# Optimization experiments

Measured on AMD Instinct MI355X. Metric: run time of the kernel, lower is better.

## Reference

```python
import jax, jax.numpy as jnp
import numpy as np

N = 8192
QS = 128
KS = 128
F = 256
EPS = 1e-5     # BatchNorm1d default eps
SLOPE = 0.01   # LeakyReLU default negative_slope


def _leaky(x):
    return jnp.where(x >= 0, x, SLOPE * x)


def _mlp_bn(x, w1, b1, w2, b2, gamma, beta):
    # Sequential(Linear, LeakyReLU, Linear, LeakyReLU) then BatchNorm1d (training mode)
    h = _leaky(x @ w1 + b1)
    h = _leaky(h @ w2 + b2)
    mean = h.mean(axis=0)
    var = h.var(axis=0)  # biased variance, as torch BN uses for normalization
    return gamma * (h - mean) * jax.lax.rsqrt(var + EPS) + beta


def setup_inputs() -> dict:
    key = jax.random.key(0)
    ks = jax.random.split(key, 24)

    def lin_w(k_, fi, fo):
        s = 1.0 / np.sqrt(fi)
        return jax.random.uniform(k_, (fi, fo), minval=-s, maxval=s, dtype=jnp.float32)

    def lin_b(k_, fi, fo):
        s = 1.0 / np.sqrt(fi)
        return jax.random.uniform(k_, (fo,), minval=-s, maxval=s, dtype=jnp.float32)

    A = (jax.random.uniform(ks[0], (N, N)) < 0.004).astype(jnp.float32)
    q = jax.random.normal(ks[1], (N, QS), dtype=jnp.float32)
    k = jax.random.normal(ks[2], (N, KS), dtype=jnp.float32)

    inp = {"A": A, "q": q, "k": k}
    i = 3
    for pre, fi in (("q", QS), ("k", KS), ("v", KS)):
        inp[pre + "_w1"] = lin_w(ks[i], fi, F); i += 1
        inp[pre + "_b1"] = lin_b(ks[i], fi, F); i += 1
        inp[pre + "_w2"] = lin_w(ks[i], F, F); i += 1
        inp[pre + "_b2"] = lin_b(ks[i], F, F); i += 1
        inp[pre + "_gamma"] = jnp.ones((F,), jnp.float32)
        inp[pre + "_beta"] = jnp.zeros((F,), jnp.float32)
    return inp


def reference(A, q, k,
              q_w1, q_b1, q_w2, q_b2, q_gamma, q_beta,
              k_w1, k_b1, k_w2, k_b2, k_gamma, k_beta,
              v_w1, v_b1, v_w2, v_b2, v_gamma, v_beta):
    qe1 = _mlp_bn(q, q_w1, q_b1, q_w2, q_b2, q_gamma, q_beta)   # [N, F]
    ke1 = _mlp_bn(k, k_w1, k_b1, k_w2, k_b2, k_gamma, k_beta)   # [N, F]
    prod = (qe1 @ ke1.T) / jnp.sqrt(jnp.float32(F))             # [N, N]
    # NOTE: faithful to source — mask zeroes scores (not -inf) before softmax
    masked = A * prod
    attn = jax.nn.softmax(masked, axis=1)
    ve1 = _mlp_bn(k, v_w1, v_b1, v_w2, v_b2, v_gamma, v_beta)   # [N, F]
    return attn @ ve1                                            # [N, F]
```

## Files before the change

kernel.cpp:

```cpp
#include <hip/hip_runtime.h>

#define NROWS 8192
#define FDIM 256
#define CAP 128

typedef _Float16 half8_t __attribute__((ext_vector_type(8)));
typedef _Float16 half4_t __attribute__((ext_vector_type(4)));
typedef float floatx4 __attribute__((ext_vector_type(4)));

struct MlpPtrs {
  const float* w1[3]; const float* b1[3];
  const float* w2[3]; const float* b2[3];
  const float* gamma[3]; const float* beta[3];
};

__global__ __launch_bounds__(256) void prep_kernel(
    const float* __restrict__ q, const float* __restrict__ k, MlpPtrs p,
    _Float16* __restrict__ qh, _Float16* __restrict__ kh,
    _Float16* __restrict__ w1p, _Float16* __restrict__ w2p) {
  int task = blockIdx.y;
  int tid = blockIdx.x * 256 + threadIdx.x;
  if (task < 2) {
    const float* src = task == 0 ? q : k;
    _Float16* dst = task == 0 ? qh : kh;
    const floatx4* s4 = (const floatx4*)src;
    half4_t* d4 = (half4_t*)dst;
    for (int idx = tid; idx < (NROWS * 128) / 4; idx += 256 * 256) {
      floatx4 v = s4[idx];
      d4[idx] = (half4_t){(_Float16)v[0], (_Float16)v[1], (_Float16)v[2], (_Float16)v[3]};
    }
    return;
  }
  int m = (task - 2) % 3;
  bool isw2 = task >= 5;
  int K = isw2 ? 256 : 128;
  if (tid >= K * 256) return;
  const float* src = isw2 ? p.w2[m] : p.w1[m];
  _Float16* dst = isw2 ? (w2p + m * 65536) : (w1p + m * 32768);
  int j = tid & 7, lane = (tid >> 3) & 63, rest = tid >> 9;
  int ktiles = K >> 5;
  int k_tile = rest % ktiles, n_tile = rest / ktiles;
  int kk = k_tile * 32 + (lane >> 4) * 8 + j;
  int nn = n_tile * 16 + (lane & 15);
  dst[tid] = (_Float16)src[kk * 256 + nn];
}

__global__ __launch_bounds__(256) void gemm1_kernel(
    const _Float16* __restrict__ qh, const _Float16* __restrict__ kh,
    const _Float16* __restrict__ w1p, MlpPtrs p, _Float16* __restrict__ h1) {
  const int mlp = blockIdx.z;
  const _Float16* X = (mlp == 0) ? qh : kh;
  const _Float16* wp = w1p + mlp * 32768;
  _Float16* out = h1 + (size_t)mlp * (NROWS * FDIM);
  const float* bias = p.b1[mlp];
  int lane = threadIdx.x & 63, wave = threadIdx.x >> 6;
  int lm = lane & 15, lq = lane >> 4;
  int m0 = blockIdx.x * 64 + wave * 16;
  int n0 = blockIdx.y * 64;
  floatx4 acc[4];
  #pragma unroll
  for (int t = 0; t < 4; ++t) acc[t] = (floatx4){0.f, 0.f, 0.f, 0.f};
  const half8_t* ap = (const half8_t*)(X + (size_t)(m0 + lm) * 128 + lq * 8);
  const half8_t* wp8 = (const half8_t*)wp;
  #pragma unroll
  for (int kt = 0; kt < 4; ++kt) {
    half8_t a = ap[kt * 4];
    #pragma unroll
    for (int t = 0; t < 4; ++t) {
      half8_t b = wp8[(((n0 >> 4) + t) * 4 + kt) * 64 + lane];
      acc[t] = __builtin_amdgcn_mfma_f32_16x16x32_f16(a, b, acc[t], 0, 0, 0);
    }
  }
  #pragma unroll
  for (int t = 0; t < 4; ++t) {
    int col = n0 + t * 16 + lm;
    float bb = bias[col];
    #pragma unroll
    for (int r = 0; r < 4; ++r) {
      float v = acc[t][r] + bb;
      v = (v >= 0.f) ? v : 0.01f * v;
      out[(size_t)(m0 + lq * 4 + r) * FDIM + col] = (_Float16)v;
    }
  }
}

__global__ __launch_bounds__(256) void gemm2_kernel(
    const _Float16* __restrict__ h1, const _Float16* __restrict__ w2p,
    MlpPtrs p, _Float16* __restrict__ e1,
    float* __restrict__ colsum, float* __restrict__ colsumsq) {
  const int mlp = blockIdx.z;
  const _Float16* X = h1 + (size_t)mlp * (NROWS * FDIM);
  const _Float16* wp = w2p + mlp * 65536;
  _Float16* out = e1 + (size_t)mlp * (NROWS * FDIM);
  const float* bias = p.b2[mlp];
  int lane = threadIdx.x & 63, wave = threadIdx.x >> 6;
  int lm = lane & 15, lq = lane >> 4;
  int m0 = blockIdx.x * 64 + wave * 16;
  int n0 = blockIdx.y * 64;
  floatx4 acc[4];
  #pragma unroll
  for (int t = 0; t < 4; ++t) acc[t] = (floatx4){0.f, 0.f, 0.f, 0.f};
  const half8_t* ap = (const half8_t*)(X + (size_t)(m0 + lm) * 256 + lq * 8);
  const half8_t* wp8 = (const half8_t*)wp;
  #pragma unroll
  for (int kt = 0; kt < 8; ++kt) {
    half8_t a = ap[kt * 4];
    #pragma unroll
    for (int t = 0; t < 4; ++t) {
      half8_t b = wp8[(((n0 >> 4) + t) * 8 + kt) * 64 + lane];
      acc[t] = __builtin_amdgcn_mfma_f32_16x16x32_f16(a, b, acc[t], 0, 0, 0);
    }
  }
  #pragma unroll
  for (int t = 0; t < 4; ++t) {
    int col = n0 + t * 16 + lm;
    float bb = bias[col];
    float s = 0.f, s2 = 0.f;
    #pragma unroll
    for (int r = 0; r < 4; ++r) {
      float v = acc[t][r] + bb;
      v = (v >= 0.f) ? v : 0.01f * v;
      out[(size_t)(m0 + lq * 4 + r) * FDIM + col] = (_Float16)v;
      s += v; s2 += v * v;
    }
    s  += __shfl_xor(s, 16, 64);  s  += __shfl_xor(s, 32, 64);
    s2 += __shfl_xor(s2, 16, 64); s2 += __shfl_xor(s2, 32, 64);
    if (lq == 0) {
      atomicAdd(&colsum[mlp * FDIM + col], s);
      atomicAdd(&colsumsq[mlp * FDIM + col], s2);
    }
  }
}

__global__ __launch_bounds__(256) void norm_kernel(
    _Float16* __restrict__ e1, const float* __restrict__ colsum,
    const float* __restrict__ colsumsq, MlpPtrs p, float* __restrict__ S_all) {
  int mlp = blockIdx.y;
  int c = threadIdx.x;
  _Float16* h = e1 + (size_t)mlp * (NROWS * FDIM);
  float mean = colsum[mlp * FDIM + c] * (1.f / NROWS);
  float var = colsumsq[mlp * FDIM + c] * (1.f / NROWS) - mean * mean;
  float scale = p.gamma[mlp][c] * rsqrtf(var + 1e-5f);
  float shift = p.beta[mlp][c] - mean * scale;
  int r0 = blockIdx.x * 32;
  float sv = 0.f;
  for (int r = 0; r < 32; ++r) {
    size_t idx = (size_t)(r0 + r) * FDIM + c;
    float v = (float)h[idx] * scale + shift;
    _Float16 hv = (_Float16)v;
    h[idx] = hv;
    sv += (float)hv;
  }
  if (mlp == 2) atomicAdd(&S_all[c], sv);
}

__global__ __launch_bounds__(256) void attn_kernel(
    const float* __restrict__ A,
    const _Float16* __restrict__ e1, const float* __restrict__ S_all,
    float* __restrict__ out) {
  const _Float16* qe = e1;
  const _Float16* ke = e1 + (size_t)1 * NROWS * FDIM;
  const _Float16* ve = e1 + (size_t)2 * NROWS * FDIM;
  int i = blockIdx.x;
  int tid = threadIdx.x, lane = tid & 63, wave = tid >> 6;
  __shared__ int sj[CAP];
  __shared__ float sw[CAP];
  __shared__ float pacc[4][FDIM];
  __shared__ int s_cnt;
  if (tid == 0) s_cnt = 0;
  __syncthreads();

  const floatx4* row = (const floatx4*)(A + (size_t)i * NROWS);
  floatx4 av[8];
  #pragma unroll
  for (int it = 0; it < 8; ++it)
    av[it] = __builtin_nontemporal_load(&row[it * 256 + tid]);
  #pragma unroll
  for (int it = 0; it < 8; ++it) {
    int v4 = it * 256 + tid;
    int cols[4]; int c = 0;
    if (av[it][0] != 0.f) cols[c++] = v4 * 4 + 0;
    if (av[it][1] != 0.f) cols[c++] = v4 * 4 + 1;
    if (av[it][2] != 0.f) cols[c++] = v4 * 4 + 2;
    if (av[it][3] != 0.f) cols[c++] = v4 * 4 + 3;
    if (c) {
      int pos = atomicAdd(&s_cnt, c);
      for (int l = 0; l < c; ++l) if (pos + l < CAP) sj[pos + l] = cols[l];
    }
  }
  __syncthreads();
  int nnz = s_cnt < CAP ? s_cnt : CAP;

  int cl = lane & 15, g = lane >> 4;
  const half8_t* qe8 = (const half8_t*)(qe + (size_t)i * FDIM + cl * 16);
  half8_t qa = qe8[0], qb = qe8[1];
  for (int e = wave * 4 + g; e < nnz; e += 16) {
    int j = sj[e];
    const half8_t* ke8 = (const half8_t*)(ke + (size_t)j * FDIM + cl * 16);
    half8_t ka = ke8[0], kb = ke8[1];
    float s = 0.f;
    #pragma unroll
    for (int r = 0; r < 8; ++r)
      s += (float)qa[r] * (float)ka[r] + (float)qb[r] * (float)kb[r];
    #pragma unroll
    for (int off = 8; off >= 1; off >>= 1) s += __shfl_xor(s, off, 64);
    if (cl == 0) sw[e] = s * 0.0625f;
  }
  __syncthreads();

  float v0 = lane < nnz ? sw[lane] : 0.f;
  float v1 = lane + 64 < nnz ? sw[lane + 64] : 0.f;
  float m = fmaxf(fmaxf(v0, v1), 0.f);
  #pragma unroll
  for (int off = 32; off >= 1; off >>= 1) m = fmaxf(m, __shfl_xor(m, off, 64));
  float em = __expf(-m);
  float w0 = lane < nnz ? __expf(v0 - m) : 0.f;
  float w1 = lane + 64 < nnz ? __expf(v1 - m) : 0.f;
  float ls = w0 + w1;
  #pragma unroll
  for (int off = 32; off >= 1; off >>= 1) ls += __shfl_xor(ls, off, 64);
  float inv = 1.f / (ls + (float)(NROWS - nnz) * em);

  int par = lane >> 5, c8 = lane & 31;
  floatx4 accA = (floatx4){0.f, 0.f, 0.f, 0.f};
  floatx4 accB = (floatx4){0.f, 0.f, 0.f, 0.f};
  for (int e = wave * 2 + par; e < nnz; e += 8) {
    int j = sj[e];
    float w = __expf(sw[e] - m) - em;
    half8_t vv = *(const half8_t*)(ve + (size_t)j * FDIM + c8 * 8);
    accA[0] += w * (float)vv[0]; accA[1] += w * (float)vv[1];
    accA[2] += w * (float)vv[2]; accA[3] += w * (float)vv[3];
    accB[0] += w * (float)vv[4]; accB[1] += w * (float)vv[5];
    accB[2] += w * (float)vv[6]; accB[3] += w * (float)vv[7];
  }
  #pragma unroll
  for (int r = 0; r < 4; ++r) {
    accA[r] += __shfl_xor(accA[r], 32, 64);
    accB[r] += __shfl_xor(accB[r], 32, 64);
  }
  if (par == 0) {
    ((floatx4*)&pacc[wave][c8 * 8])[0] = accA;
    ((floatx4*)&pacc[wave][c8 * 8])[1] = accB;
  }
  __syncthreads();

  int c = tid;
  float s = pacc[0][c] + pacc[1][c] + pacc[2][c] + pacc[3][c] + em * S_all[c];
  __builtin_nontemporal_store(s * inv, &out[(size_t)i * FDIM + c]);
}

extern "C" void kernel_launch(void* const* d_in, const int* in_sizes, int n_in,
                              void* d_out, int out_size, void* d_ws, size_t ws_size,
                              hipStream_t stream) {
  const float* A = (const float*)d_in[0];
  const float* q = (const float*)d_in[1];
  const float* k = (const float*)d_in[2];
  MlpPtrs p;
  for (int m = 0; m < 3; ++m) {
    const int b = 3 + m * 6;
    p.w1[m]    = (const float*)d_in[b + 0];
    p.b1[m]    = (const float*)d_in[b + 1];
    p.w2[m]    = (const float*)d_in[b + 2];
    p.b2[m]    = (const float*)d_in[b + 3];
    p.gamma[m] = (const float*)d_in[b + 4];
    p.beta[m]  = (const float*)d_in[b + 5];
  }
  char* ws = (char*)d_ws;
  const size_t MB = 1024 * 1024;
  _Float16* qh  = (_Float16*)(ws + 0);
  _Float16* kh  = (_Float16*)(ws + 2 * MB);
  _Float16* h1  = (_Float16*)(ws + 4 * MB);
  _Float16* e1  = (_Float16*)(ws + 16 * MB);
  _Float16* w1p = (_Float16*)(ws + 28 * MB);
  _Float16* w2p = (_Float16*)(ws + 28 * MB + 192 * 1024);
  float* colsum   = (float*)(ws + 28 * MB + 640 * 1024);
  float* colsumsq = colsum + 3 * FDIM;
  float* S_all    = colsumsq + 3 * FDIM;

  (void)hipMemsetAsync(colsum, 0, 7 * 1024, stream);
  prep_kernel<<<dim3(256, 8, 1), 256, 0, stream>>>(q, k, p, qh, kh, w1p, w2p);
  gemm1_kernel<<<dim3(128, 4, 3), 256, 0, stream>>>(qh, kh, w1p, p, h1);
  gemm2_kernel<<<dim3(128, 4, 3), 256, 0, stream>>>(h1, w2p, p, e1, colsum, colsumsq);
  norm_kernel<<<dim3(256, 3, 1), 256, 0, stream>>>(e1, colsum, colsumsq, p, S_all);
  attn_kernel<<<NROWS, 256, 0, stream>>>(A, e1, S_all, (float*)d_out);
}
```

Baseline: 458.0 us.

## Fold BatchNorm affine into attention and assign one row per wave

Drops the separate norm pass that rewrote all three embeddings. Instead a tiny stats kernel computes per-column scale and shift, which the attention kernel applies algebraically: scaled q times k-scale in the score, and v's affine applied after aggregation using colsum. The fp32-to-fp16 conversion of q and k moves into gemm1's loads, removing the staging copy. Attention now processes one row per wave with no block-level syncs. This trades extra per-row arithmetic and fp16-rounding differences from unnormalized values for less memory traffic and fewer launches.

After: 456.0 us (median of 2 runs). No clear change (-0.4%).

```diff
diff --git a/kernel.cpp b/kernel.cpp
--- a/kernel.cpp
+++ b/kernel.cpp
@@ -15,24 +15,11 @@
 };
 
 __global__ __launch_bounds__(256) void prep_kernel(
-    const float* __restrict__ q, const float* __restrict__ k, MlpPtrs p,
-    _Float16* __restrict__ qh, _Float16* __restrict__ kh,
-    _Float16* __restrict__ w1p, _Float16* __restrict__ w2p) {
+    MlpPtrs p, _Float16* __restrict__ w1p, _Float16* __restrict__ w2p) {
   int task = blockIdx.y;
   int tid = blockIdx.x * 256 + threadIdx.x;
-  if (task < 2) {
-    const float* src = task == 0 ? q : k;
-    _Float16* dst = task == 0 ? qh : kh;
-    const floatx4* s4 = (const floatx4*)src;
-    half4_t* d4 = (half4_t*)dst;
-    for (int idx = tid; idx < (NROWS * 128) / 4; idx += 256 * 256) {
-      floatx4 v = s4[idx];
-      d4[idx] = (half4_t){(_Float16)v[0], (_Float16)v[1], (_Float16)v[2], (_Float16)v[3]};
-    }
-    return;
-  }
-  int m = (task - 2) % 3;
-  bool isw2 = task >= 5;
+  int m = task % 3;
+  bool isw2 = task >= 3;
   int K = isw2 ? 256 : 128;
   if (tid >= K * 256) return;
   const float* src = isw2 ? p.w2[m] : p.w1[m];
@@ -46,10 +33,10 @@
 }
 
 __global__ __launch_bounds__(256) void gemm1_kernel(
-    const _Float16* __restrict__ qh, const _Float16* __restrict__ kh,
+    const float* __restrict__ q, const float* __restrict__ k,
     const _Float16* __restrict__ w1p, MlpPtrs p, _Float16* __restrict__ h1) {
   const int mlp = blockIdx.z;
-  const _Float16* X = (mlp == 0) ? qh : kh;
+  const float* X = (mlp == 0) ? q : k;
   const _Float16* wp = w1p + mlp * 32768;
   _Float16* out = h1 + (size_t)mlp * (NROWS * FDIM);
   const float* bias = p.b1[mlp];
@@ -60,11 +47,14 @@
   floatx4 acc[4];
   #pragma unroll
   for (int t = 0; t < 4; ++t) acc[t] = (floatx4){0.f, 0.f, 0.f, 0.f};
-  const half8_t* ap = (const half8_t*)(X + (size_t)(m0 + lm) * 128 + lq * 8);
+  const float* ap = X + (size_t)(m0 + lm) * 128 + lq * 8;
   const half8_t* wp8 = (const half8_t*)wp;
   #pragma unroll
   for (int kt = 0; kt < 4; ++kt) {
-    half8_t a = ap[kt * 4];
+    floatx4 a0 = *(const floatx4*)(ap + kt * 32);
+    floatx4 a1 = *(const floatx4*)(ap + kt * 32 + 4);
+    half8_t a = (half8_t){(_Float16)a0[0], (_Float16)a0[1], (_Float16)a0[2], (_Float16)a0[3],
+                          (_Float16)a1[0], (_Float16)a1[1], (_Float16)a1[2], (_Float16)a1[3]};
     #pragma unroll
     for (int t = 0; t < 4; ++t) {
       half8_t b = wp8[(((n0 >> 4) + t) * 4 + kt) * 64 + lane];
@@ -132,84 +122,92 @@
   }
 }
 
-__global__ __launch_bounds__(256) void norm_kernel(
-    _Float16* __restrict__ e1, const float* __restrict__ colsum,
-    const float* __restrict__ colsumsq, MlpPtrs p, float* __restrict__ S_all) {
-  int mlp = blockIdx.y;
+__global__ __launch_bounds__(256) void stats_kernel(
+    const float* __restrict__ colsum, const float* __restrict__ colsumsq,
+    MlpPtrs p, float* __restrict__ scaleA, float* __restrict__ shiftA) {
   int c = threadIdx.x;
-  _Float16* h = e1 + (size_t)mlp * (NROWS * FDIM);
-  float mean = colsum[mlp * FDIM + c] * (1.f / NROWS);
-  float var = colsumsq[mlp * FDIM + c] * (1.f / NROWS) - mean * mean;
-  float scale = p.gamma[mlp][c] * rsqrtf(var + 1e-5f);
-  float shift = p.beta[mlp][c] - mean * scale;
-  int r0 = blockIdx.x * 32;
-  float sv = 0.f;
-  for (int r = 0; r < 32; ++r) {
-    size_t idx = (size_t)(r0 + r) * FDIM + c;
-    float v = (float)h[idx] * scale + shift;
-    _Float16 hv = (_Float16)v;
-    h[idx] = hv;
-    sv += (float)hv;
-  }
-  if (mlp == 2) atomicAdd(&S_all[c], sv);
+  #pragma unroll
+  for (int m = 0; m < 3; ++m) {
+    float mean = colsum[m * FDIM + c] * (1.f / NROWS);
+    float var = colsumsq[m * FDIM + c] * (1.f / NROWS) - mean * mean;
+    float sc = p.gamma[m][c] * rsqrtf(var + 1e-5f);
+    scaleA[m * FDIM + c] = sc;
+    shiftA[m * FDIM + c] = p.beta[m][c] - mean * sc;
+  }
 }
 
 __global__ __launch_bounds__(256) void attn_kernel(
-    const float* __restrict__ A,
-    const _Float16* __restrict__ e1, const float* __restrict__ S_all,
-    float* __restrict__ out) {
+    const float* __restrict__ A, const _Float16* __restrict__ e1,
+    const float* __restrict__ scaleA, const float* __restrict__ shiftA,
+    const float* __restrict__ colsum, float* __restrict__ out) {
   const _Float16* qe = e1;
   const _Float16* ke = e1 + (size_t)1 * NROWS * FDIM;
   const _Float16* ve = e1 + (size_t)2 * NROWS * FDIM;
-  int i = blockIdx.x;
-  int tid = threadIdx.x, lane = tid & 63, wave = tid >> 6;
-  __shared__ int sj[CAP];
-  __shared__ float sw[CAP];
-  __shared__ float pacc[4][FDIM];
-  __shared__ int s_cnt;
-  if (tid == 0) s_cnt = 0;
-  __syncthreads();
+  int lane = threadIdx.x & 63, wave = threadIdx.x >> 6;
+  int i = blockIdx.x * 4 + wave;
+  __shared__ int sj[4][CAP];
+  __shared__ float sw[4][CAP];
+  __shared__ int cnt[4];
+  if (lane == 0) cnt[wave] = 0;
 
   const floatx4* row = (const floatx4*)(A + (size_t)i * NROWS);
-  floatx4 av[8];
-  #pragma unroll
-  for (int it = 0; it < 8; ++it)
-    av[it] = __builtin_nontemporal_load(&row[it * 256 + tid]);
-  #pragma unroll
-  for (int it = 0; it < 8; ++it) {
-    int v4 = it * 256 + tid;
-    int cols[4]; int c = 0;
-    if (av[it][0] != 0.f) cols[c++] = v4 * 4 + 0;
-    if (av[it][1] != 0.f) cols[c++] = v4 * 4 + 1;
-    if (av[it][2] != 0.f) cols[c++] = v4 * 4 + 2;
-    if (av[it][3] != 0.f) cols[c++] = v4 * 4 + 3;
-    if (c) {
-      int pos = atomicAdd(&s_cnt, c);
-      for (int l = 0; l < c; ++l) if (pos + l < CAP) sj[pos + l] = cols[l];
-    }
-  }
-  __syncthreads();
-  int nnz = s_cnt < CAP ? s_cnt : CAP;
+  for (int b = 0; b < 4; ++b) {
+    floatx4 av[8];
+    #pragma unroll
+    for (int it = 0; it < 8; ++it)
+      av[it] = __builtin_nontemporal_load(&row[(b * 8 + it) * 64 + lane]);
+    #pragma unroll
+    for (int it = 0; it < 8; ++it) {
+      int base = ((b * 8 + it) * 64 + lane) * 4;
+      int cols[4]; int c = 0;
+      if (av[it][0] != 0.f) cols[c++] = base + 0;
+      if (av[it][1] != 0.f) cols[c++] = base + 1;
+      if (av[it][2] != 0.f) cols[c++] = base + 2;
+      if (av[it][3] != 0.f) cols[c++] = base + 3;
+      if (c) {
+        int pos = atomicAdd(&cnt[wave], c);
+        for (int l = 0; l < c; ++l) if (pos + l < CAP) sj[wave][pos + l] = cols[l];
+      }
+    }
+  }
+  int nnz = cnt[wave] < CAP ? cnt[wave] : CAP;
 
   int cl = lane & 15, g = lane >> 4;
-  const half8_t* qe8 = (const half8_t*)(qe + (size_t)i * FDIM + cl * 16);
-  half8_t qa = qe8[0], qb = qe8[1];
-  for (int e = wave * 4 + g; e < nnz; e += 16) {
-    int j = sj[e];
-    const half8_t* ke8 = (const half8_t*)(ke + (size_t)j * FDIM + cl * 16);
-    half8_t ka = ke8[0], kb = ke8[1];
-    float s = 0.f;
+  const half8_t* qp = (const half8_t*)(qe + (size_t)i * FDIM + cl * 16);
+  half8_t qa = qp[0], qb8 = qp[1];
+  const floatx4* sq4 = (const floatx4*)(scaleA + cl * 16);
+  const floatx4* hq4 = (const floatx4*)(shiftA + cl * 16);
+  const floatx4* sk4 = (const floatx4*)(scaleA + FDIM + cl * 16);
+  const floatx4* hk4 = (const floatx4*)(shiftA + FDIM + cl * 16);
+  float qk[16]; float qb = 0.f;
+  #pragma unroll
+  for (int v4 = 0; v4 < 4; ++v4) {
+    floatx4 sq = sq4[v4], hq = hq4[v4], sk = sk4[v4], hk = hk4[v4];
+    #pragma unroll
+    for (int r = 0; r < 4; ++r) {
+      int c = v4 * 4 + r;
+      float qr = (c < 8) ? (float)qa[c] : (float)qb8[c - 8];
+      float qn = qr * sq[r] + hq[r];
+      qk[c] = qn * sk[r] * 0.0625f;
+      qb += qn * hk[r] * 0.0625f;
+    }
+  }
+
+  for (int e = g; e < nnz; e += 4) {
+    int j = sj[wave][e];
+    const half8_t* kp = (const half8_t*)(ke + (size_t)j * FDIM + cl * 16);
+    half8_t ka = kp[0], kb = kp[1];
+    float s = qb;
     #pragma unroll
     for (int r = 0; r < 8; ++r)
-      s += (float)qa[r] * (float)ka[r] + (float)qb[r] * (float)kb[r];
+      s += qk[r] * (float)ka[r] + qk[r + 8] * (float)kb[r];
     #pragma unroll
     for (int off = 8; off >= 1; off >>= 1) s += __shfl_xor(s, off, 64);
-    if (cl == 0) sw[e] = s * 0.0625f;
-  }
-  __syncthreads();
-
-  float v0 = lane < nnz ? sw[lane] : 0.f;
-  float v1 = lane + 64 < nnz ? sw[lane + 64] : 0.f;
+    if (cl == 0) sw[wave][e] = s;
+  }
+
+  float v0 = lane < nnz ? sw[wave][lane] : 0.f;
+  float v1 = lane + 64 < nnz ? sw[wave][lane + 64] : 0.f;
   float m = fmaxf(fmaxf(v0, v1), 0.f);
   #pragma unroll
   for (int off = 32; off >= 1; off >>= 1) m = fmaxf(m, __shfl_xor(m, off, 64));
@@ -219,34 +217,29 @@
   float ls = w0 + w1;
   #pragma unroll
   for (int off = 32; off >= 1; off >>= 1) ls += __shfl_xor(ls, off, 64);
+  if (lane < nnz) sw[wave][lane] = w0 - em;
+  if (lane + 64 < nnz) sw[wave][lane + 64] = w1 - em;
+  float wsum = ls - (float)nnz * em;
   float inv = 1.f / (ls + (float)(NROWS - nnz) * em);
 
-  int par = lane >> 5, c8 = lane & 31;
-  floatx4 accA = (floatx4){0.f, 0.f, 0.f, 0.f};
-  floatx4 accB = (floatx4){0.f, 0.f, 0.f, 0.f};
-  for (int e = wave * 2 + par; e < nnz; e += 8) {
-    int j = sj[e];
-    float w = __expf(sw[e] - m) - em;
-    half8_t vv = *(const half8_t*)(ve + (size_t)j * FDIM + c8 * 8);
-    accA[0] += w * (float)vv[0]; accA[1] += w * (float)vv[1];
-    accA[2] += w * (float)vv[2]; accA[3] += w * (float)vv[3];
-    accB[0] += w * (float)vv[4]; accB[1] += w * (float)vv[5];
-    accB[2] += w * (float)vv[6]; accB[3] += w * (float)vv[7];
-  }
-  #pragma unroll
-  for (int r = 0; r < 4; ++r) {
-    accA[r] += __shfl_xor(accA[r], 32, 64);
-    accB[r] += __shfl_xor(accB[r], 32, 64);
-  }
-  if (par == 0) {
-    ((floatx4*)&pacc[wave][c8 * 8])[0] = accA;
-    ((floatx4*)&pacc[wave][c8 * 8])[1] = accB;
-  }
-  __syncthreads();
-
-  int c = tid;
-  float s = pacc[0][c] + pacc[1][c] + pacc[2][c] + pacc[3][c] + em * S_all[c];
-  __builtin_nontemporal_store(s * inv, &out[(size_t)i * FDIM + c]);
+  floatx4 acc = (floatx4){0.f, 0.f, 0.f, 0.f};
+  for (int e = 0; e < nnz; ++e) {
+    int j = sj[wave][e];
+    float w = sw[wave][e];
+    half4_t vv = *(const half4_t*)(ve + (size_t)j * FDIM + lane * 4);
+    acc[0] += w * (float)vv[0]; acc[1] += w * (float)vv[1];
+    acc[2] += w * (float)vv[2]; acc[3] += w * (float)vv[3];
+  }
+
+  floatx4 sv = *(const floatx4*)(scaleA + 2 * FDIM + lane * 4);
+  floatx4 sh = *(const floatx4*)(shiftA + 2 * FDIM + lane * 4);
+  floatx4 cs = *(const floatx4*)(colsum + 2 * FDIM + lane * 4);
+  float bg = wsum + em * (float)NROWS;
+  floatx4 o;
+  #pragma unroll
+  for (int r = 0; r < 4; ++r)
+    o[r] = inv * (sv[r] * (acc[r] + em * cs[r]) + sh[r] * bg);
+  __builtin_nontemporal_store(o, (floatx4*)(out + (size_t)i * FDIM + lane * 4));
 }
 
 extern "C" void kernel_launch(void* const* d_in, const int* in_sizes, int n_in,
@@ -267,20 +260,19 @@
   }
   char* ws = (char*)d_ws;
   const size_t MB = 1024 * 1024;
-  _Float16* qh  = (_Float16*)(ws + 0);
-  _Float16* kh  = (_Float16*)(ws + 2 * MB);
-  _Float16* h1  = (_Float16*)(ws + 4 * MB);
-  _Float16* e1  = (_Float16*)(ws + 16 * MB);
-  _Float16* w1p = (_Float16*)(ws + 28 * MB);
-  _Float16* w2p = (_Float16*)(ws + 28 * MB + 192 * 1024);
-  float* colsum   = (float*)(ws + 28 * MB + 640 * 1024);
+  _Float16* h1  = (_Float16*)(ws + 0);
+  _Float16* e1  = (_Float16*)(ws + 12 * MB);
+  _Float16* w1p = (_Float16*)(ws + 24 * MB);
+  _Float16* w2p = (_Float16*)(ws + 24 * MB + 192 * 1024);
+  float* colsum   = (float*)(ws + 25 * MB);
   float* colsumsq = colsum + 3 * FDIM;
-  float* S_all    = colsumsq + 3 * FDIM;
-
-  (void)hipMemsetAsync(colsum, 0, 7 * 1024, stream);
-  prep_kernel<<<dim3(256, 8, 1), 256, 0, stream>>>(q, k, p, qh, kh, w1p, w2p);
-  gemm1_kernel<<<dim3(128, 4, 3), 256, 0, stream>>>(qh, kh, w1p, p, h1);
+  float* scaleA   = colsumsq + 3 * FDIM;
+  float* shiftA   = scaleA + 3 * FDIM;
+
+  (void)hipMemsetAsync(colsum, 0, 2 * 3 * FDIM * sizeof(float), stream);
+  prep_kernel<<<dim3(256, 6, 1), 256, 0, stream>>>(p, w1p, w2p);
+  gemm1_kernel<<<dim3(128, 4, 3), 256, 0, stream>>>(q, k, w1p, p, h1);
   gemm2_kernel<<<dim3(128, 4, 3), 256, 0, stream>>>(h1, w2p, p, e1, colsum, colsumsq);
-  norm_kernel<<<dim3(256, 3, 1), 256, 0, stream>>>(e1, colsum, colsumsq, p, S_all);
-  attn_kernel<<<NROWS, 256, 0, stream>>>(A, e1, S_all, (float*)d_out);
-}
+  stats_kernel<<<1, 256, 0, stream>>>(colsum, colsumsq, p, scaleA, shiftA);
+  attn_kernel<<<NROWS / 4, 256, 0, stream>>>(A, e1, scaleA, shiftA, colsum, (float*)d_out);
+}
```
